# Performance work log

Hardware: AMD Instinct MI355X
Metric: run time of the kernel (lower is better)

## Reference

```python
import jax, jax.numpy as jnp
import numpy as np

N, E, IN, OUT, ED = 100000, 1600000, 64, 64, 16
NEG = -1000000000.0


def setup_inputs() -> dict:
    key = jax.random.key(0)
    ks = jax.random.split(key, 8)
    x = jax.random.normal(ks[0], (N, IN), jnp.float32)
    edge_index = jax.random.randint(ks[1], (2, E), 0, N, dtype=jnp.int32)
    edge_attr = jax.random.normal(ks[2], (E, ED), jnp.float32)
    # xavier-ish init for linear weights (stored as [in, out] for x @ W)
    Wn = jax.random.normal(ks[3], (IN, OUT), jnp.float32) * (1.0 / np.sqrt(IN))
    We = jax.random.normal(ks[4], (ED, OUT), jnp.float32) * (1.0 / np.sqrt(ED))
    att_src = jax.random.normal(ks[5], (OUT,), jnp.float32) * 0.02
    att_dst = jax.random.normal(ks[6], (OUT,), jnp.float32) * 0.02
    att_edge = jax.random.normal(ks[7], (OUT,), jnp.float32) * 0.02
    return {"x": x, "edge_index": edge_index, "edge_attr": edge_attr,
            "Wn": Wn, "We": We, "att_src": att_src, "att_dst": att_dst,
            "att_edge": att_edge}


def reference(x, edge_index, edge_attr, Wn, We, att_src, att_dst, att_edge):
    src, dst = edge_index[0], edge_index[1]
    n = x.shape[0]
    z = x @ Wn                      # [N, OUT]
    e = edge_attr @ We              # [E, OUT]
    # per-edge attention logits
    s_src = (z @ att_src)[src]      # [E]
    s_dst = (z @ att_dst)[dst]      # [E]
    s_edge = e @ att_edge           # [E]
    score = jax.nn.leaky_relu(s_src + s_dst + s_edge, negative_slope=0.2)
    # scatter softmax over dst segments (stable; matches torch amax with -1e9 init)
    max_per = jnp.maximum(jax.ops.segment_max(score, dst, num_segments=n), NEG)
    score_exp = jnp.exp(score - max_per[dst])
    denom = jax.ops.segment_sum(score_exp, dst, num_segments=n)
    alpha = score_exp / (denom[dst] + 1e-8)   # [E]
    # message + scatter-add aggregation; dropout is identity (p=0 / eval)
    msg = (z[src] + e) * alpha[:, None]       # [E, OUT]
    out = jax.ops.segment_sum(msg, dst, num_segments=n)
    # residual: in_dim == out_dim -> Identity
    return out + x
```

## Files before the change

kernel.cpp:

```cpp
#include <hip/hip_runtime.h>
#include <hip/hip_bf16.h>
#include <math.h>


__device__ __forceinline__ float bf2f(unsigned short u) {
  return __uint_as_float(((unsigned)u) << 16);
}
__device__ __forceinline__ float rdlane(float v, int k) {
  return __uint_as_float(
      (unsigned)__builtin_amdgcn_readlane((int)__float_as_uint(v), k));
}
__device__ __forceinline__ float wave_sum64(float v) {
#pragma unroll
  for (int o = 32; o > 0; o >>= 1) v += __shfl_xor(v, o);
  return v;
}

__global__ __launch_bounds__(256) void k_init(const float* __restrict__ We,
                                              const float* __restrict__ att_edge,
                                              float* __restrict__ weA,
                                              int* __restrict__ total,
                                              int* __restrict__ count, int n) {
  int i = blockIdx.x * 256 + threadIdx.x;
  for (int j = i; j < n; j += gridDim.x * 256) count[j] = 0;
  if (blockIdx.x == 0) {
    int t = threadIdx.x;
    if (t < 16) {
      float a = 0.f;
#pragma unroll
      for (int c = 0; c < 64; ++c) a = fmaf(We[t * 64 + c], att_edge[c], a);
      weA[t] = a;
    }
    if (t == 16) *total = 0;
  }
}

__global__ __launch_bounds__(256) void k_nodecnt(
    const float* __restrict__ x, const float* __restrict__ Wn,
    const float* __restrict__ att_src, const float* __restrict__ att_dst,
    unsigned short* __restrict__ zb, float* __restrict__ zs,
    float* __restrict__ zd, int n, const int* __restrict__ dst,
    int* __restrict__ count, int* __restrict__ pos, int e, int nbn) {
  if ((int)blockIdx.x < nbn) {
    const int lane = threadIdx.x & 63;
    const int wid = (blockIdx.x * 256 + threadIdx.x) >> 6;
    const int nw = nbn * 4;
    float wn[64];
#pragma unroll
    for (int k = 0; k < 64; ++k) wn[k] = Wn[k * 64 + lane];
    const float as = att_src[lane], ad = att_dst[lane];
    for (int r = wid; r < n; r += nw) {
      float xv = x[(size_t)r * 64 + lane];
      float a0 = 0.f, a1 = 0.f, a2 = 0.f, a3 = 0.f;
#pragma unroll
      for (int k = 0; k < 64; k += 4) {
        a0 = fmaf(__shfl(xv, k), wn[k], a0);
        a1 = fmaf(__shfl(xv, k + 1), wn[k + 1], a1);
        a2 = fmaf(__shfl(xv, k + 2), wn[k + 2], a2);
        a3 = fmaf(__shfl(xv, k + 3), wn[k + 3], a3);
      }
      float acc = (a0 + a1) + (a2 + a3);
      __hip_bfloat16 b = __float2bfloat16(acc);
      zb[(size_t)r * 64 + lane] = *reinterpret_cast<unsigned short*>(&b);
      float ps = wave_sum64(acc * as);
      float pd = wave_sum64(acc * ad);
      if (lane == 0) {
        zs[r] = ps;
        zd[r] = pd;
      }
    }
  } else {
    int i = (blockIdx.x - nbn) * 256 + threadIdx.x;
    const int stride = (gridDim.x - nbn) * 256;
    for (; i < e; i += stride) pos[i] = atomicAdd(&count[dst[i]], 1);
  }
}

__global__ __launch_bounds__(256) void k_offsets(const int* __restrict__ count,
                                                 int* __restrict__ start,
                                                 int* __restrict__ total, int n) {
  __shared__ int sdata[256];
  __shared__ int sbase;
  const int tid = threadIdx.x;
  const int i = blockIdx.x * 256 + tid;
  int c = (i < n) ? count[i] : 0;
  int v = c;
  sdata[tid] = v;
  __syncthreads();
  for (int off = 1; off < 256; off <<= 1) {
    int t = (tid >= off) ? sdata[tid - off] : 0;
    __syncthreads();
    v += t;
    sdata[tid] = v;
    __syncthreads();
  }
  if (tid == 255) sbase = atomicAdd(total, v);
  __syncthreads();
  if (i < n) start[i] = sbase + (v - c);
}

__global__ __launch_bounds__(256) void k_scatter(
    const int* __restrict__ src, const int* __restrict__ dst,
    const int* __restrict__ pos, const float* __restrict__ zs,
    const float* __restrict__ zd, const float* __restrict__ ea,
    const float* __restrict__ weA, const int* __restrict__ start,
    uint4* __restrict__ es, int e) {
  int i = blockIdx.x * 256 + threadIdx.x;
  if (i >= e) return;
  int s = src[i], d = dst[i], p = pos[i];
  size_t slot = (size_t)start[d] + p;
  const float4* eap = (const float4*)(ea + (size_t)i * 16);
  float4 q0 = eap[0], q1 = eap[1], q2 = eap[2], q3 = eap[3];
  float sed = q0.x * weA[0] + q0.y * weA[1] + q0.z * weA[2] + q0.w * weA[3] +
              q1.x * weA[4] + q1.y * weA[5] + q1.z * weA[6] + q1.w * weA[7] +
              q2.x * weA[8] + q2.y * weA[9] + q2.z * weA[10] + q2.w * weA[11] +
              q3.x * weA[12] + q3.y * weA[13] + q3.z * weA[14] + q3.w * weA[15];
  float sv = zs[s] + zd[d] + sed;
  float sc = (sv > 0.f) ? sv : 0.2f * sv;
  es[slot] = make_uint4((unsigned)s, __float_as_uint(sc), (unsigned)i, 0u);
}

__global__ __launch_bounds__(256) void k_agg(
    const float* __restrict__ x, const unsigned short* __restrict__ zb,
    const float* __restrict__ ea, const float* __restrict__ We,
    const int* __restrict__ start, const int* __restrict__ count,
    const uint4* __restrict__ es, float* __restrict__ out, int n) {
  const int lane = threadIdx.x & 63;
  const int grp = lane >> 4;
  const int gl = lane & 15;
  const int nw = (gridDim.x * blockDim.x) >> 6;
  int d = (blockIdx.x * blockDim.x + threadIdx.x) >> 6;
  if (d >= n) return;

  int s0 = start[d], cnt = count[d];
  while (d < n) {
    int dn = d + nw, sn0 = 0, cn = 0;
    if (dn < n) {
      sn0 = start[dn];
      cn = count[dn];
    }

    const int q0 = (cnt * grp) >> 2;
    const int q1 = (cnt * (grp + 1)) >> 2;

    float gm = -1e30f;
    for (int t = q0; t < q1; ++t)
      gm = fmaxf(gm, __uint_as_float(es[(size_t)s0 + t].y));
    gm = fmaxf(gm, __shfl_xor(gm, 16));
    gm = fmaxf(gm, __shfl_xor(gm, 32));
    const float m = gm;

    float dsum = 0.f, ag = 0.f;
    float4 msg = make_float4(0.f, 0.f, 0.f, 0.f);
    int t = q0;
    for (; t + 2 <= q1; t += 2) {
      uint4 h0 = es[(size_t)s0 + t];
      uint4 h1 = es[(size_t)s0 + t + 1];
      float w0 = __expf(__uint_as_float(h0.y) - m);
      float w1 = __expf(__uint_as_float(h1.y) - m);
      ushort4 z0 = *(const ushort4*)(zb + (size_t)h0.x * 64 + gl * 4);
      ushort4 z1 = *(const ushort4*)(zb + (size_t)h1.x * 64 + gl * 4);
      float a0 = ea[(size_t)h0.z * 16 + gl];
      float a1 = ea[(size_t)h1.z * 16 + gl];
      dsum += w0 + w1;
      msg.x = fmaf(w0, bf2f(z0.x), fmaf(w1, bf2f(z1.x), msg.x));
      msg.y = fmaf(w0, bf2f(z0.y), fmaf(w1, bf2f(z1.y), msg.y));
      msg.z = fmaf(w0, bf2f(z0.z), fmaf(w1, bf2f(z1.z), msg.z));
      msg.w = fmaf(w0, bf2f(z0.w), fmaf(w1, bf2f(z1.w), msg.w));
      ag = fmaf(w0, a0, fmaf(w1, a1, ag));
    }
    if (t < q1) {
      uint4 h0 = es[(size_t)s0 + t];
      float w0 = __expf(__uint_as_float(h0.y) - m);
      ushort4 z0 = *(const ushort4*)(zb + (size_t)h0.x * 64 + gl * 4);
      float a0 = ea[(size_t)h0.z * 16 + gl];
      dsum += w0;
      msg.x = fmaf(w0, bf2f(z0.x), msg.x);
      msg.y = fmaf(w0, bf2f(z0.y), msg.y);
      msg.z = fmaf(w0, bf2f(z0.z), msg.z);
      msg.w = fmaf(w0, bf2f(z0.w), msg.w);
      ag = fmaf(w0, a0, ag);
    }

    dsum += __shfl_xor(dsum, 16);
    dsum += __shfl_xor(dsum, 32);
    msg.x += __shfl_xor(msg.x, 16); msg.x += __shfl_xor(msg.x, 32);
    msg.y += __shfl_xor(msg.y, 16); msg.y += __shfl_xor(msg.y, 32);
    msg.z += __shfl_xor(msg.z, 16); msg.z += __shfl_xor(msg.z, 32);
    msg.w += __shfl_xor(msg.w, 16); msg.w += __shfl_xor(msg.w, 32);
    ag += __shfl_xor(ag, 16);
    ag += __shfl_xor(ag, 32);

    const float4* We4 = (const float4*)We;
    float4 evec = make_float4(0.f, 0.f, 0.f, 0.f);
#pragma unroll
    for (int k = 0; k < 16; ++k) {
      float agk = rdlane(ag, k);
      float4 wef = We4[k * 16 + gl];
      evec.x = fmaf(agk, wef.x, evec.x);
      evec.y = fmaf(agk, wef.y, evec.y);
      evec.z = fmaf(agk, wef.z, evec.z);
      evec.w = fmaf(agk, wef.w, evec.w);
    }

    if (grp == 0) {
      float inv = 1.f / (dsum + 1e-8f);
      const float4 xr = *(const float4*)(x + (size_t)d * 64 + gl * 4);
      float4 r;
      r.x = fmaf(msg.x + evec.x, inv, xr.x);
      r.y = fmaf(msg.y + evec.y, inv, xr.y);
      r.z = fmaf(msg.z + evec.z, inv, xr.z);
      r.w = fmaf(msg.w + evec.w, inv, xr.w);
      *(float4*)(out + (size_t)d * 64 + gl * 4) = r;
    }

    d = dn; s0 = sn0; cnt = cn;
  }
}

extern "C" void kernel_launch(void* const* d_in, const int* in_sizes, int n_in,
                              void* d_out, int out_size, void* d_ws, size_t ws_size,
                              hipStream_t stream) {
  const float* x = (const float*)d_in[0];
  const int* ei = (const int*)d_in[1];
  const float* ea = (const float*)d_in[2];
  const float* Wn = (const float*)d_in[3];
  const float* We = (const float*)d_in[4];
  const float* att_src = (const float*)d_in[5];
  const float* att_dst = (const float*)d_in[6];
  const float* att_edge = (const float*)d_in[7];
  float* out = (float*)d_out;

  const int N = in_sizes[0] / 64;
  const int E = in_sizes[1] / 2;
  const int* src = ei;
  const int* dst = ei + E;

  char* p = (char*)d_ws;
  auto carve = [&](size_t bytes) {
    void* q = (void*)p;
    p += (bytes + 255) & ~(size_t)255;
    return q;
  };
  unsigned short* zb = (unsigned short*)carve((size_t)N * 64 * 2);
  float* zs = (float*)carve((size_t)N * sizeof(float));
  float* zd = (float*)carve((size_t)N * sizeof(float));
  int* count = (int*)carve((size_t)N * sizeof(int));
  int* startp = (int*)carve((size_t)N * sizeof(int));
  int* pos = (int*)carve((size_t)E * sizeof(int));
  float* weA = (float*)carve(64);
  int* total = (int*)carve(64);
  uint4* es = (uint4*)carve((size_t)E * 16);

  k_init<<<256, 256, 0, stream>>>(We, att_edge, weA, total, count, N);
  k_nodecnt<<<4096, 256, 0, stream>>>(x, Wn, att_src, att_dst, zb, zs, zd, N,
                                      dst, count, pos, E, 2048);
  k_offsets<<<(N + 255) / 256, 256, 0, stream>>>(count, startp, total, N);
  k_scatter<<<(E + 255) / 256, 256, 0, stream>>>(src, dst, pos, zs, zd, ea, weA,
                                                 startp, es, E);
  k_agg<<<4096, 256, 0, stream>>>(x, zb, ea, We, startp, count, es, out, N);
}
```

Measured before the change: 284.6 us.

## Precompute Wn·att vectors and split node GEMM from score/count kernel

Folds att_src/att_dst into Wn once (vs = Wn·att_src, vd = Wn·att_dst), so per-node source and destination scores become 64-wide dot products with x, computed alongside the dst counting atomics. The full x@Wn bf16 projection moves to its own kernel that reads x rows through wave-uniform loads instead of lane shuffles. This drops the per-row wave reductions and shuffles, but adds a kernel launch and reads x twice. The algebraic reassociation slightly changes rounding of the scores.

```diff
diff --git a/kernel.cpp b/kernel.cpp
--- a/kernel.cpp
+++ b/kernel.cpp
@@ -10,69 +10,89 @@
   return __uint_as_float(
       (unsigned)__builtin_amdgcn_readlane((int)__float_as_uint(v), k));
 }
-__device__ __forceinline__ float wave_sum64(float v) {
-#pragma unroll
-  for (int o = 32; o > 0; o >>= 1) v += __shfl_xor(v, o);
-  return v;
-}
-
-__global__ __launch_bounds__(256) void k_init(const float* __restrict__ We,
-                                              const float* __restrict__ att_edge,
-                                              float* __restrict__ weA,
-                                              int* __restrict__ total,
-                                              int* __restrict__ count, int n) {
+
+__global__ __launch_bounds__(256) void k_init(
+    const float* __restrict__ Wn, const float* __restrict__ We,
+    const float* __restrict__ att_src, const float* __restrict__ att_dst,
+    const float* __restrict__ att_edge, float* __restrict__ vs,
+    float* __restrict__ vd, float* __restrict__ weA, int* __restrict__ total,
+    int* __restrict__ count, int n) {
   int i = blockIdx.x * 256 + threadIdx.x;
   for (int j = i; j < n; j += gridDim.x * 256) count[j] = 0;
   if (blockIdx.x == 0) {
     int t = threadIdx.x;
-    if (t < 16) {
+    if (t < 64) {
+      float a = 0.f, b = 0.f;
+#pragma unroll
+      for (int c = 0; c < 64; ++c) {
+        a = fmaf(Wn[t * 64 + c], att_src[c], a);
+        b = fmaf(Wn[t * 64 + c], att_dst[c], b);
+      }
+      vs[t] = a;
+      vd[t] = b;
+    } else if (t < 80) {
       float a = 0.f;
 #pragma unroll
-      for (int c = 0; c < 64; ++c) a = fmaf(We[t * 64 + c], att_edge[c], a);
-      weA[t] = a;
-    }
-    if (t == 16) *total = 0;
-  }
-}
-
-__global__ __launch_bounds__(256) void k_nodecnt(
-    const float* __restrict__ x, const float* __restrict__ Wn,
-    const float* __restrict__ att_src, const float* __restrict__ att_dst,
-    unsigned short* __restrict__ zb, float* __restrict__ zs,
-    float* __restrict__ zd, int n, const int* __restrict__ dst,
-    int* __restrict__ count, int* __restrict__ pos, int e, int nbn) {
-  if ((int)blockIdx.x < nbn) {
-    const int lane = threadIdx.x & 63;
-    const int wid = (blockIdx.x * 256 + threadIdx.x) >> 6;
-    const int nw = nbn * 4;
-    float wn[64];
-#pragma unroll
-    for (int k = 0; k < 64; ++k) wn[k] = Wn[k * 64 + lane];
-    const float as = att_src[lane], ad = att_dst[lane];
-    for (int r = wid; r < n; r += nw) {
-      float xv = x[(size_t)r * 64 + lane];
-      float a0 = 0.f, a1 = 0.f, a2 = 0.f, a3 = 0.f;
-#pragma unroll
-      for (int k = 0; k < 64; k += 4) {
-        a0 = fmaf(__shfl(xv, k), wn[k], a0);
-        a1 = fmaf(__shfl(xv, k + 1), wn[k + 1], a1);
-        a2 = fmaf(__shfl(xv, k + 2), wn[k + 2], a2);
-        a3 = fmaf(__shfl(xv, k + 3), wn[k + 3], a3);
-      }
-      float acc = (a0 + a1) + (a2 + a3);
-      __hip_bfloat16 b = __float2bfloat16(acc);
-      zb[(size_t)r * 64 + lane] = *reinterpret_cast<unsigned short*>(&b);
-      float ps = wave_sum64(acc * as);
-      float pd = wave_sum64(acc * ad);
-      if (lane == 0) {
-        zs[r] = ps;
-        zd[r] = pd;
-      }
-    }
+      for (int c = 0; c < 64; ++c) a = fmaf(We[(t - 64) * 64 + c], att_edge[c], a);
+      weA[t - 64] = a;
+    } else if (t == 80) {
+      *total = 0;
+    }
+  }
+}
+
+__global__ __launch_bounds__(256) void k_cntzs(
+    const int* __restrict__ dst, int* __restrict__ count, int* __restrict__ pos,
+    int e, const float* __restrict__ x, const float* __restrict__ vs,
+    const float* __restrict__ vd, float* __restrict__ zs,
+    float* __restrict__ zd, int n, int nbe) {
+  if ((int)blockIdx.x < nbe) {
+    int i = blockIdx.x * 256 + threadIdx.x;
+    const int stride = nbe * 256;
+    for (; i < e; i += stride) pos[i] = atomicAdd(&count[dst[i]], 1);
   } else {
-    int i = (blockIdx.x - nbn) * 256 + threadIdx.x;
-    const int stride = (gridDim.x - nbn) * 256;
-    for (; i < e; i += stride) pos[i] = atomicAdd(&count[dst[i]], 1);
+    int r = (blockIdx.x - nbe) * 256 + threadIdx.x;
+    if (r >= n) return;
+    const float4* xr = (const float4*)(x + (size_t)r * 64);
+    const float4* vs4 = (const float4*)vs;
+    const float4* vd4 = (const float4*)vd;
+    float s = 0.f, d = 0.f;
+#pragma unroll
+    for (int j = 0; j < 16; ++j) {
+      float4 q = xr[j];
+      float4 a = vs4[j], b = vd4[j];
+      s = fmaf(q.x, a.x, fmaf(q.y, a.y, fmaf(q.z, a.z, fmaf(q.w, a.w, s))));
+      d = fmaf(q.x, b.x, fmaf(q.y, b.y, fmaf(q.z, b.z, fmaf(q.w, b.w, d))));
+    }
+    zs[r] = s;
+    zd[r] = d;
+  }
+}
+
+__global__ __launch_bounds__(256) void k_gemm(const float* __restrict__ x,
+                                              const float* __restrict__ Wn,
+                                              unsigned short* __restrict__ zb,
+                                              int n) {
+  const int lane = threadIdx.x & 63;
+  const int wid = (blockIdx.x * 256 + threadIdx.x) >> 6;
+  const int nw = gridDim.x * 4;
+  float wn[64];
+#pragma unroll
+  for (int k = 0; k < 64; ++k) wn[k] = Wn[k * 64 + lane];
+  for (int r = wid; r < n; r += nw) {
+    const int ru = __builtin_amdgcn_readfirstlane(r);
+    const float* xr = x + (size_t)ru * 64;
+    float a0 = 0.f, a1 = 0.f, a2 = 0.f, a3 = 0.f;
+#pragma unroll
+    for (int k = 0; k < 64; k += 4) {
+      a0 = fmaf(xr[k], wn[k], a0);
+      a1 = fmaf(xr[k + 1], wn[k + 1], a1);
+      a2 = fmaf(xr[k + 2], wn[k + 2], a2);
+      a3 = fmaf(xr[k + 3], wn[k + 3], a3);
+    }
+    float acc = (a0 + a1) + (a2 + a3);
+    __hip_bfloat16 b = __float2bfloat16(acc);
+    zb[(size_t)ru * 64 + lane] = *reinterpret_cast<unsigned short*>(&b);
   }
 }
 
@@ -249,12 +269,18 @@
   int* startp = (int*)carve((size_t)N * sizeof(int));
   int* pos = (int*)carve((size_t)E * sizeof(int));
   float* weA = (float*)carve(64);
+  float* vs = (float*)carve(256);
+  float* vd = (float*)carve(256);
   int* total = (int*)carve(64);
   uint4* es = (uint4*)carve((size_t)E * 16);
 
-  k_init<<<256, 256, 0, stream>>>(We, att_edge, weA, total, count, N);
-  k_nodecnt<<<4096, 256, 0, stream>>>(x, Wn, att_src, att_dst, zb, zs, zd, N,
-                                      dst, count, pos, E, 2048);
+  const int nbe = 2048;
+  const int nbn = (N + 255) / 256;
+  k_init<<<256, 256, 0, stream>>>(Wn, We, att_src, att_dst, att_edge, vs, vd,
+                                  weA, total, count, N);
+  k_cntzs<<<nbe + nbn, 256, 0, stream>>>(dst, count, pos, E, x, vs, vd, zs, zd,
+                                         N, nbe);
+  k_gemm<<<2048, 256, 0, stream>>>(x, Wn, zb, N);
   k_offsets<<<(N + 255) / 256, 256, 0, stream>>>(count, startp, total, N);
   k_scatter<<<(E + 255) / 256, 256, 0, stream>>>(src, dst, pos, zs, zd, ea, weA,
                                                  startp, es, E);
```

Measured after the change: 261.5 us. -8.1%, faster.
